# Kernel tuning notes

Measured on AMD Instinct MI355X. Metric: run time of the kernel, lower is better.

Reference implementation:

```python
import jax, jax.numpy as jnp
import numpy as np

B, T, IN = 32, 1024, 256
H = 128          # hidden_size
NL = 2           # num_layers
NC = 4           # num_classes
F2 = 2 * H       # bidirectional feature size


def _lstm_dir(xs, w_ih, w_hh, b_ih, b_hh, reverse):
    # xs: [T, B, in]; w_ih: [4H, in]; w_hh: [4H, H]
    if reverse:
        xs = xs[::-1]
    h0 = jnp.zeros((xs.shape[1], H), xs.dtype)
    c0 = jnp.zeros((xs.shape[1], H), xs.dtype)

    def step(carry, xt):
        h, c = carry
        g = xt @ w_ih.T + b_ih + h @ w_hh.T + b_hh  # [B, 4H]
        i, f, gg, o = jnp.split(g, 4, axis=-1)       # PyTorch gate order i,f,g,o
        c = jax.nn.sigmoid(f) * c + jax.nn.sigmoid(i) * jnp.tanh(gg)
        h = jax.nn.sigmoid(o) * jnp.tanh(c)
        return (h, c), h

    _, hs = jax.lax.scan(step, (h0, c0), xs)  # [T, B, H]
    if reverse:
        hs = hs[::-1]
    return hs


def setup_inputs() -> dict:
    key = jax.random.key(0)
    ks = jax.random.split(key, 12)
    s = 0.05
    x = jax.random.normal(ks[0], (B, T, IN), jnp.float32)
    # stacked LSTM params: [layer, direction, ...]; layer0 in = IN, layer1 in = 2H = IN
    w_ih = jax.random.normal(ks[1], (NL, 2, 4 * H, IN), jnp.float32) * s
    w_hh = jax.random.normal(ks[2], (NL, 2, 4 * H, H), jnp.float32) * s
    b_ih = jax.random.normal(ks[3], (NL, 2, 4 * H), jnp.float32) * s
    b_hh = jax.random.normal(ks[4], (NL, 2, 4 * H), jnp.float32) * s
    wq = jax.random.normal(ks[5], (F2, F2), jnp.float32) * s
    wk = jax.random.normal(ks[6], (F2, F2), jnp.float32) * s
    wv = jax.random.normal(ks[7], (F2, F2), jnp.float32) * s
    bq = jax.random.normal(ks[8], (F2,), jnp.float32) * s
    bk = jax.random.normal(ks[9], (F2,), jnp.float32) * s
    bv = jax.random.normal(ks[10], (F2,), jnp.float32) * s
    w_fc = jax.random.normal(ks[11], (NC, F2), jnp.float32) * s
    b_fc = jnp.zeros((NC,), jnp.float32)
    return {"x": x, "w_ih": w_ih, "w_hh": w_hh, "b_ih": b_ih, "b_hh": b_hh,
            "wq": wq, "wk": wk, "wv": wv, "bq": bq, "bk": bk, "bv": bv,
            "w_fc": w_fc, "b_fc": b_fc}


def reference(x, w_ih, w_hh, b_ih, b_hh, wq, wk, wv, bq, bk, bv, w_fc, b_fc):
    # --- biLSTM (eval mode: inter-layer dropout inactive) ---
    xs = jnp.swapaxes(x, 0, 1)  # time-major [T, B, IN]
    for l in range(NL):
        fwd = _lstm_dir(xs, w_ih[l, 0], w_hh[l, 0], b_ih[l, 0], b_hh[l, 0], False)
        bwd = _lstm_dir(xs, w_ih[l, 1], w_hh[l, 1], b_ih[l, 1], b_hh[l, 1], True)
        xs = jnp.concatenate([fwd, bwd], axis=-1)  # [T, B, 2H]
    out = jnp.swapaxes(xs, 0, 1)  # [B, T, 2H]
    # --- naive full self-attention ---
    q = out @ wq.T + bq
    k = out @ wk.T + bk
    v = out @ wv.T + bv
    scores = jnp.einsum('btd,bsd->bts', q, k) / jnp.sqrt(jnp.float32(F2))
    attn = jax.nn.softmax(scores, axis=-1)          # [B, T, T]
    ctx = jnp.einsum('bts,bsd->btd', attn, v)       # [B, T, 2H]
    # --- FC head on last timestep ---
    return ctx[:, -1, :] @ w_fc.T + b_fc            # [B, NC]
```

## Files before the change

kernel.cpp:

```cpp
#include <hip/hip_runtime.h>
#include <math.h>
#include <stdint.h>

#define BB 32
#define TT 1024
#define HH 128
#define G4 512
#define CH 16
#define XPS 516

typedef _Float16 half2_t __attribute__((ext_vector_type(2)));
typedef _Float16 half8_t __attribute__((ext_vector_type(8)));
typedef float f32x4 __attribute__((ext_vector_type(4)));

__device__ __forceinline__ float fdot2f(half2_t a, half2_t b, float c) {
    return __builtin_amdgcn_fdot2(a, b, c, false);
}
__device__ __forceinline__ float rcpf(float x) {
    return __builtin_amdgcn_rcpf(x);
}
__device__ __forceinline__ float dpp_xor1(float x) {
    return __builtin_bit_cast(float, __builtin_amdgcn_update_dpp(
        0, __builtin_bit_cast(int, x), 0xB1, 0xF, 0xF, true));
}
__device__ __forceinline__ float dpp_xor2(float x) {
    return __builtin_bit_cast(float, __builtin_amdgcn_update_dpp(
        0, __builtin_bit_cast(int, x), 0x4E, 0xF, 0xF, true));
}
__device__ __forceinline__ void bar_lgkm() {
    asm volatile("s_waitcnt lgkmcnt(0)\n\ts_barrier" ::: "memory");
}

__global__ __launch_bounds__(256) void cvt_wih(
    const float* __restrict__ w, _Float16* __restrict__ o)
{
    const int i = (blockIdx.x * 256 + threadIdx.x) * 4;
    float4 f = *(const float4*)(w + i);
    half2_t t[2] = { half2_t{(_Float16)f.x, (_Float16)f.y},
                     half2_t{(_Float16)f.z, (_Float16)f.w} };
    *(float2*)(o + i) = *(float2*)t;
}

__global__ __launch_bounds__(512, 1) void lstm_fused(
    const float* __restrict__ x_in,
    const _Float16* __restrict__ wih16_l,
    const float* __restrict__ b_ih_l,
    const float* __restrict__ b_hh_l,
    const float* __restrict__ w_hh_l,
    float* __restrict__ out)
{
    const int b = blockIdx.x & 31;
    const int d = blockIdx.x >> 5;
    const int tid = threadIdx.x;
    const int wvid = tid >> 6;
    const int l = tid & 63;
    const int s = l & 3;
    const int g = l >> 2;
    const int j = (wvid << 4) | g;

    __shared__ __align__(16) _Float16 hs[HH];
    __shared__ __align__(16) float xp[2][CH * XPS];
    __shared__ __align__(16) half2_t xr[2][CH * 128];
    __shared__ __align__(16) float obuf[CH * HH];

    half2_t wv[4][16];
#pragma unroll
    for (int G = 0; G < 4; ++G) {
        const float* wr = w_hh_l + (size_t)(d * G4 + 128 * G + j) * HH + 32 * s;
#pragma unroll
        for (int q4 = 0; q4 < 8; ++q4) {
            float4 f = *(const float4*)(wr + 4 * q4);
            wv[G][2 * q4]     = half2_t{(_Float16)f.x, (_Float16)f.y};
            wv[G][2 * q4 + 1] = half2_t{(_Float16)f.z, (_Float16)f.w};
        }
    }

    const int acol0 = wvid * 64 + (l & 15);
    const _Float16* wn = wih16_l + ((size_t)d * G4 + acol0) * 256 + (l >> 4) * 8;
    const float bias0 = b_ih_l[d * G4 + acol0]      + b_hh_l[d * G4 + acol0];
    const float bias1 = b_ih_l[d * G4 + acol0 + 16] + b_hh_l[d * G4 + acol0 + 16];
    const float bias2 = b_ih_l[d * G4 + acol0 + 32] + b_hh_l[d * G4 + acol0 + 32];
    const float bias3 = b_ih_l[d * G4 + acol0 + 48] + b_hh_l[d * G4 + acol0 + 48];

    const int cbase = ((acol0 & 127) << 2) + (acol0 >> 7);

    const float* xbase = x_in + (size_t)b * TT * 256;

    const int a_noswz = (l & 15) * 512 + (l >> 4) * 16;
    const int a_swz   = (l & 7) << 4;
    const int w_swz_byte = (tid * 16) ^ (((tid >> 5) & 7) << 4);

#pragma unroll 1
    for (int p = 0; p < 2; ++p) {
        const int tlo = d ? (1008 - p * CH) : p * CH;
        const float* gs = xbase + (size_t)tlo * 256 + tid * 8;
        float4 f0 = *(const float4*)gs;
        float4 f1 = *(const float4*)(gs + 4);
        half2_t t4[4] = { half2_t{(_Float16)f0.x, (_Float16)f0.y},
                          half2_t{(_Float16)f0.z, (_Float16)f0.w},
                          half2_t{(_Float16)f1.x, (_Float16)f1.y},
                          half2_t{(_Float16)f1.z, (_Float16)f1.w} };
        *(float4*)((char*)xr[p] + w_swz_byte) = *(float4*)t4;
    }
    __syncthreads();

    f32x4 acc0 = {bias0, bias0, bias0, bias0};
    f32x4 acc1 = {bias1, bias1, bias1, bias1};
    f32x4 acc2 = {bias2, bias2, bias2, bias2};
    f32x4 acc3 = {bias3, bias3, bias3, bias3};

#pragma unroll
    for (int kt = 0; kt < 8; ++kt) {
        half8_t af = *(const half8_t*)((const char*)xr[0] + ((a_noswz + kt * 64) ^ a_swz));
        acc0 = __builtin_amdgcn_mfma_f32_16x16x32_f16(af, *(const half8_t*)(wn +         kt * 32), acc0, 0, 0, 0);
        acc1 = __builtin_amdgcn_mfma_f32_16x16x32_f16(af, *(const half8_t*)(wn +  4096 + kt * 32), acc1, 0, 0, 0);
        acc2 = __builtin_amdgcn_mfma_f32_16x16x32_f16(af, *(const half8_t*)(wn +  8192 + kt * 32), acc2, 0, 0, 0);
        acc3 = __builtin_amdgcn_mfma_f32_16x16x32_f16(af, *(const half8_t*)(wn + 12288 + kt * 32), acc3, 0, 0, 0);
    }
    {
        const int rb = (l >> 4) * 4;
#pragma unroll
        for (int q = 0; q < 4; ++q) {
            const int ix = (rb + q) * XPS + cbase;
            xp[0][ix]       = acc0[q];
            xp[0][ix + 64]  = acc1[q];
            xp[0][ix + 128] = acc2[q];
            xp[0][ix + 192] = acc3[q];
        }
    }
    acc0 = (f32x4){bias0, bias0, bias0, bias0};
    acc1 = (f32x4){bias1, bias1, bias1, bias1};
    acc2 = (f32x4){bias2, bias2, bias2, bias2};
    acc3 = (f32x4){bias3, bias3, bias3, bias3};

    if (tid < 64) ((half2_t*)hs)[tid] = half2_t{(_Float16)0.f, (_Float16)0.f};
    float c = 0.f;
    float* ob = out + (size_t)b * TT * 256 + d * HH;
    __syncthreads();

    float4 rg0 = {}, rg1 = {};
    for (int ck = 0; ck < 64; ++ck) {
        const int cur = ck & 1;
        const bool doproj = (ck + 1 < 64);
        if (ck + 2 < 64) {
            const int tlo2 = d ? (1008 - (ck + 2) * CH) : (ck + 2) * CH;
            const float* gs = xbase + (size_t)tlo2 * 256 + tid * 8;
            rg0 = *(const float4*)gs;
            rg1 = *(const float4*)(gs + 4);
        }
        const float* xb = xp[cur];
        const char* xr_rd = (const char*)xr[cur ^ 1];

        auto rec_step = [&](int si) {
            const int lds_t = d ? (CH - 1 - si) : si;
            const float4 xg4 = *(const float4*)&xb[lds_t * XPS + (j << 2)];

            const float4* hp = (const float4*)(hs + 32 * s);
            float4 hA = hp[0], hB = hp[1], hC = hp[2], hD = hp[3];
            half2_t hh[16];
            hh[0]  = __builtin_bit_cast(half2_t, hA.x);
            hh[1]  = __builtin_bit_cast(half2_t, hA.y);
            hh[2]  = __builtin_bit_cast(half2_t, hA.z);
            hh[3]  = __builtin_bit_cast(half2_t, hA.w);
            hh[4]  = __builtin_bit_cast(half2_t, hB.x);
            hh[5]  = __builtin_bit_cast(half2_t, hB.y);
            hh[6]  = __builtin_bit_cast(half2_t, hB.z);
            hh[7]  = __builtin_bit_cast(half2_t, hB.w);
            hh[8]  = __builtin_bit_cast(half2_t, hC.x);
            hh[9]  = __builtin_bit_cast(half2_t, hC.y);
            hh[10] = __builtin_bit_cast(half2_t, hC.z);
            hh[11] = __builtin_bit_cast(half2_t, hC.w);
            hh[12] = __builtin_bit_cast(half2_t, hD.x);
            hh[13] = __builtin_bit_cast(half2_t, hD.y);
            hh[14] = __builtin_bit_cast(half2_t, hD.z);
            hh[15] = __builtin_bit_cast(half2_t, hD.w);

            float a0 = 0.f, a1 = 0.f, a2 = 0.f, a3 = 0.f;
            float e0 = 0.f, e1 = 0.f, e2 = 0.f, e3 = 0.f;
#pragma unroll
            for (int kk = 0; kk < 8; ++kk) {
                a0 = fdot2f(wv[0][kk], hh[kk], a0);
                a1 = fdot2f(wv[1][kk], hh[kk], a1);
                a2 = fdot2f(wv[2][kk], hh[kk], a2);
                a3 = fdot2f(wv[3][kk], hh[kk], a3);
                e0 = fdot2f(wv[0][kk + 8], hh[kk + 8], e0);
                e1 = fdot2f(wv[1][kk + 8], hh[kk + 8], e1);
                e2 = fdot2f(wv[2][kk + 8], hh[kk + 8], e2);
                e3 = fdot2f(wv[3][kk + 8], hh[kk + 8], e3);
            }
            a0 += e0; a1 += e1; a2 += e2; a3 += e3;

            a0 += dpp_xor1(a0); a0 += dpp_xor2(a0);
            a1 += dpp_xor1(a1); a1 += dpp_xor2(a1);
            a2 += dpp_xor1(a2); a2 += dpp_xor2(a2);
            a3 += dpp_xor1(a3); a3 += dpp_xor2(a3);

            const float gi = rcpf(1.f + __expf(-(a0 + xg4.x)));
            const float gf = rcpf(1.f + __expf(-(a1 + xg4.y)));
            const float gg = 1.f - 2.f * rcpf(1.f + __expf(2.f * (a2 + xg4.z)));
            const float go = rcpf(1.f + __expf(-(a3 + xg4.w)));
            c = gf * c + gi * gg;
            const float th = 1.f - 2.f * rcpf(1.f + __expf(2.f * c));
            const float h = go * th;
            if (s == 0) {
                hs[j] = (_Float16)h;
                obuf[si * HH + j] = h;
            }
        };

        half8_t gbEA = {}, gbEB = {}, gbOA = {}, gbOB = {};
        if (doproj) {
            gbEA = *(const half8_t*)(wn);
            gbEB = *(const half8_t*)(wn + 4096);
        }

#pragma unroll 1
        for (int sp = 0; sp < CH / 2; ++sp) {
            const int kt = sp;
            half8_t afrag = {};
            if (doproj) {
                afrag = *(const half8_t*)(xr_rd + ((a_noswz + kt * 64) ^ a_swz));
                gbOA = *(const half8_t*)(wn +  8192 + kt * 32);
                gbOB = *(const half8_t*)(wn + 12288 + kt * 32);
            }
            rec_step(2 * sp);
            if (doproj) {
                acc0 = __builtin_amdgcn_mfma_f32_16x16x32_f16(afrag, gbEA, acc0, 0, 0, 0);
                acc1 = __builtin_amdgcn_mfma_f32_16x16x32_f16(afrag, gbEB, acc1, 0, 0, 0);
            }
            bar_lgkm();
            if (doproj) {
                const int ktn = (kt + 1) & 7;
                gbEA = *(const half8_t*)(wn +        ktn * 32);
                gbEB = *(const half8_t*)(wn + 4096 + ktn * 32);
            }
            rec_step(2 * sp + 1);
            if (doproj) {
                acc2 = __builtin_amdgcn_mfma_f32_16x16x32_f16(afrag, gbOA, acc2, 0, 0, 0);
                acc3 = __builtin_amdgcn_mfma_f32_16x16x32_f16(afrag, gbOB, acc3, 0, 0, 0);
            }
            bar_lgkm();
        }

        {
            const int idx = tid * 4;
            const int sf = idx >> 7, jf = idx & 127;
            const int sg = ck * CH + sf;
            const int t  = d ? (TT - 1 - sg) : sg;
            float4 o0 = *(const float4*)&obuf[idx];
            *(float4*)&ob[(size_t)t * 256 + jf] = o0;
        }
        if (doproj) {
            float* xpn = xp[cur ^ 1];
            const int rb = (l >> 4) * 4;
#pragma unroll
            for (int q = 0; q < 4; ++q) {
                const int ix = (rb + q) * XPS + cbase;
                xpn[ix]       = acc0[q];
                xpn[ix + 64]  = acc1[q];
                xpn[ix + 128] = acc2[q];
                xpn[ix + 192] = acc3[q];
            }
            acc0 = (f32x4){bias0, bias0, bias0, bias0};
            acc1 = (f32x4){bias1, bias1, bias1, bias1};
            acc2 = (f32x4){bias2, bias2, bias2, bias2};
            acc3 = (f32x4){bias3, bias3, bias3, bias3};
        }
        if (ck + 2 < 64) {
            half2_t t4[4] = { half2_t{(_Float16)rg0.x, (_Float16)rg0.y},
                              half2_t{(_Float16)rg0.z, (_Float16)rg0.w},
                              half2_t{(_Float16)rg1.x, (_Float16)rg1.y},
                              half2_t{(_Float16)rg1.z, (_Float16)rg1.w} };
            *(float4*)((char*)xr[cur] + w_swz_byte) = *(float4*)t4;
        }
        __syncthreads();
    }
}


__global__ __launch_bounds__(256) void attn_qr(
    const float* __restrict__ out1, const float* __restrict__ wq,
    const float* __restrict__ bq,   const float* __restrict__ wk,
    float* __restrict__ r_ws, float* __restrict__ ctxw, float* __restrict__ den)
{
    const int b = blockIdx.x;
    const int tid = threadIdx.x;
    __shared__ float xl[256], q[256];
    const float* ob = out1 + (size_t)b * TT * 256;

    xl[tid] = ob[(size_t)(TT - 1) * 256 + tid];
    ctxw[b * 256 + tid] = 0.f;
    if (tid == 0) den[b] = 0.f;
    __syncthreads();

    float acc = bq[tid];
    const float* wqr = wq + (size_t)tid * 256;
#pragma unroll 4
    for (int k = 0; k < 256; ++k) acc += xl[k] * wqr[k];
    q[tid] = acc;
    __syncthreads();

    acc = 0.f;
#pragma unroll 4
    for (int dd = 0; dd < 256; ++dd) acc += q[dd] * wk[(size_t)dd * 256 + tid];
    r_ws[b * 256 + tid] = acc * 0.0625f;
}

__global__ __launch_bounds__(256) void attn_sc(
    const float* __restrict__ out1, const float* __restrict__ r_ws,
    float* __restrict__ ctxw, float* __restrict__ den)
{
    const int b  = blockIdx.x >> 3;
    const int s8 = blockIdx.x & 7;
    const int tid = threadIdx.x;
    __shared__ __align__(16) float r[256];
    __shared__ float ev[128];
    __shared__ float red[256];

    const float* ob = out1 + (size_t)b * TT * 256 + (size_t)s8 * 128 * 256;
    r[tid] = r_ws[b * 256 + tid];
    __syncthreads();

    const int wave = tid >> 6, lane = tid & 63;
    float4 r4 = *(const float4*)&r[lane * 4];
    for (int t = wave; t < 128; t += 4) {
        float4 o4 = *(const float4*)(ob + (size_t)t * 256 + lane * 4);
        float p = r4.x * o4.x + r4.y * o4.y + r4.z * o4.z + r4.w * o4.w;
#pragma unroll
        for (int off = 32; off > 0; off >>= 1) p += __shfl_down(p, off, 64);
        if (lane == 0) ev[t] = expf(p);
    }
    __syncthreads();

    red[tid] = (tid < 128) ? ev[tid] : 0.f;
    __syncthreads();
    for (int st = 128; st > 0; st >>= 1) {
        if (tid < st) red[tid] += red[tid + st];
        __syncthreads();
    }
    if (tid == 0) atomicAdd(&den[b], red[0]);

    float a = 0.f;
#pragma unroll 4
    for (int t = 0; t < 128; ++t) a += ev[t] * ob[(size_t)t * 256 + tid];
    atomicAdd(&ctxw[b * 256 + tid], a);
}

__global__ __launch_bounds__(256) void attn_fc(
    const float* __restrict__ ctxw, const float* __restrict__ den,
    const float* __restrict__ wv,   const float* __restrict__ bv,
    const float* __restrict__ wfc,  const float* __restrict__ bfc,
    float* __restrict__ outp)
{
    const int b = blockIdx.x;
    const int tid = threadIdx.x;
    __shared__ float u[256], cx[256];

    u[tid] = ctxw[b * 256 + tid] / den[b];
    __syncthreads();

    float acc = bv[tid];
    const float* wr = wv + (size_t)tid * 256;
#pragma unroll 4
    for (int k = 0; k < 256; ++k) acc += u[k] * wr[k];
    cx[tid] = acc;
    __syncthreads();

    if (tid < 4) {
        float o = bfc[tid];
        for (int k = 0; k < 256; ++k) o += cx[k] * wfc[tid * 256 + k];
        outp[b * 4 + tid] = o;
    }
}

extern "C" void kernel_launch(void* const* d_in, const int* in_sizes, int n_in,
                              void* d_out, int out_size, void* d_ws, size_t ws_size,
                              hipStream_t stream)
{
    const float* x    = (const float*)d_in[0];
    const float* w_ih = (const float*)d_in[1];
    const float* w_hh = (const float*)d_in[2];
    const float* b_ih = (const float*)d_in[3];
    const float* b_hh = (const float*)d_in[4];
    const float* wq   = (const float*)d_in[5];
    const float* wk   = (const float*)d_in[6];
    const float* wv   = (const float*)d_in[7];
    const float* bq   = (const float*)d_in[8];
    const float* bv   = (const float*)d_in[10];
    const float* wfc  = (const float*)d_in[11];
    const float* bfcv = (const float*)d_in[12];
    float* outp = (float*)d_out;

    float* ws = (float*)d_ws;
    _Float16* wih16 = (_Float16*)ws;
    float* out0 = ws + 262144;
    float* out1 = out0 + 8388608;
    float* r_ws = out1 + 8388608;
    float* ctxw = r_ws + 8192;
    float* den  = ctxw + 8192;

    cvt_wih<<<512, 256, 0, stream>>>(w_ih, wih16);

    lstm_fused<<<64, 512, 0, stream>>>(x, wih16, b_ih, b_hh, w_hh, out0);
    lstm_fused<<<64, 512, 0, stream>>>(out0, wih16 + 262144, b_ih + 1024, b_hh + 1024,
                                       w_hh + 2 * 512 * 128, out1);

    attn_qr<<<32, 256, 0, stream>>>(out1, wq, bq, wk, r_ws, ctxw, den);
    attn_sc<<<256, 256, 0, stream>>>(out1, r_ws, ctxw, den);
    attn_fc<<<32, 256, 0, stream>>>(ctxw, den, wv, bv, wfc, bfcv, outp);
}
```

Before: 1.679 ms.

## Fuse attention kernels into one launch with last-block completion counter

Merges the three attention kernels (query/key projection, score+weighted sum, value/FC head) into a single kernel. Each of the 8 blocks per batch recomputes the q·Wk vector redundantly, and the last block to finish, detected via an atomic counter, runs the value projection and FC head. Zero-initialisation of the accumulators moves into the weight conversion kernel. This removes two kernel launches and their gaps, at the cost of 8x redundant projection work per batch and reliance on threadfence/atomic ordering.

```diff
diff --git a/kernel.cpp b/kernel.cpp
--- a/kernel.cpp
+++ b/kernel.cpp
@@ -32,13 +32,16 @@
 }
 
 __global__ __launch_bounds__(256) void cvt_wih(
-    const float* __restrict__ w, _Float16* __restrict__ o)
+    const float* __restrict__ w, _Float16* __restrict__ o,
+    float* __restrict__ ctxw, float* __restrict__ den, int* __restrict__ cnt)
 {
     const int i = (blockIdx.x * 256 + threadIdx.x) * 4;
     float4 f = *(const float4*)(w + i);
     half2_t t[2] = { half2_t{(_Float16)f.x, (_Float16)f.y},
                      half2_t{(_Float16)f.z, (_Float16)f.w} };
     *(float2*)(o + i) = *(float2*)t;
+    if (blockIdx.x < 32) ctxw[blockIdx.x * 256 + threadIdx.x] = 0.f;
+    if (blockIdx.x == 32 && threadIdx.x < 32) { den[threadIdx.x] = 0.f; cnt[threadIdx.x] = 0; }
 }
 
 __global__ __launch_bounds__(512, 1) void lstm_fused(
@@ -277,58 +280,51 @@
     }
 }
 
-
-__global__ __launch_bounds__(256) void attn_qr(
-    const float* __restrict__ out1, const float* __restrict__ wq,
-    const float* __restrict__ bq,   const float* __restrict__ wk,
-    float* __restrict__ r_ws, float* __restrict__ ctxw, float* __restrict__ den)
+__global__ __launch_bounds__(256) void attn_all(
+    const float* __restrict__ out1,
+    const float* __restrict__ wq, const float* __restrict__ bq,
+    const float* __restrict__ wk,
+    const float* __restrict__ wv, const float* __restrict__ bv,
+    const float* __restrict__ wfc, const float* __restrict__ bfc,
+    float* __restrict__ ctxw, float* __restrict__ den, int* __restrict__ cnt,
+    float* __restrict__ outp)
 {
-    const int b = blockIdx.x;
+    const int b  = blockIdx.x >> 3;
+    const int s8 = blockIdx.x & 7;
     const int tid = threadIdx.x;
     __shared__ float xl[256], q[256];
-    const float* ob = out1 + (size_t)b * TT * 256;
-
-    xl[tid] = ob[(size_t)(TT - 1) * 256 + tid];
-    ctxw[b * 256 + tid] = 0.f;
-    if (tid == 0) den[b] = 0.f;
-    __syncthreads();
-
+    __shared__ __align__(16) float r[256];
+    __shared__ float ev[128];
+    __shared__ float red[256];
+    __shared__ int lastflag;
+
+    const float* obase = out1 + (size_t)b * TT * 256;
+
+    xl[tid] = obase[(size_t)(TT - 1) * 256 + tid];
+    __syncthreads();
     float acc = bq[tid];
     const float* wqr = wq + (size_t)tid * 256;
 #pragma unroll 4
     for (int k = 0; k < 256; ++k) acc += xl[k] * wqr[k];
     q[tid] = acc;
     __syncthreads();
-
     acc = 0.f;
 #pragma unroll 4
     for (int dd = 0; dd < 256; ++dd) acc += q[dd] * wk[(size_t)dd * 256 + tid];
-    r_ws[b * 256 + tid] = acc * 0.0625f;
-}
-
-__global__ __launch_bounds__(256) void attn_sc(
-    const float* __restrict__ out1, const float* __restrict__ r_ws,
-    float* __restrict__ ctxw, float* __restrict__ den)
-{
-    const int b  = blockIdx.x >> 3;
-    const int s8 = blockIdx.x & 7;
-    const int tid = threadIdx.x;
-    __shared__ __align__(16) float r[256];
-    __shared__ float ev[128];
-    __shared__ float red[256];
-
-    const float* ob = out1 + (size_t)b * TT * 256 + (size_t)s8 * 128 * 256;
-    r[tid] = r_ws[b * 256 + tid];
-    __syncthreads();
-
-    const int wave = tid >> 6, lane = tid & 63;
-    float4 r4 = *(const float4*)&r[lane * 4];
-    for (int t = wave; t < 128; t += 4) {
-        float4 o4 = *(const float4*)(ob + (size_t)t * 256 + lane * 4);
-        float p = r4.x * o4.x + r4.y * o4.y + r4.z * o4.z + r4.w * o4.w;
-#pragma unroll
-        for (int off = 32; off > 0; off >>= 1) p += __shfl_down(p, off, 64);
-        if (lane == 0) ev[t] = expf(p);
+    r[tid] = acc * 0.0625f;
+    __syncthreads();
+
+    const float* ob = obase + (size_t)s8 * 128 * 256;
+    {
+        const int wave = tid >> 6, lane = tid & 63;
+        float4 r4 = *(const float4*)&r[lane * 4];
+        for (int t = wave; t < 128; t += 4) {
+            float4 o4 = *(const float4*)(ob + (size_t)t * 256 + lane * 4);
+            float p = r4.x * o4.x + r4.y * o4.y + r4.z * o4.z + r4.w * o4.w;
+#pragma unroll
+            for (int off = 32; off > 0; off >>= 1) p += __shfl_down(p, off, 64);
+            if (lane == 0) ev[t] = expf(p);
+        }
     }
     __syncthreads();
 
@@ -340,35 +336,38 @@
     }
     if (tid == 0) atomicAdd(&den[b], red[0]);
 
-    float a = 0.f;
+    acc = 0.f;
 #pragma unroll 4
-    for (int t = 0; t < 128; ++t) a += ev[t] * ob[(size_t)t * 256 + tid];
-    atomicAdd(&ctxw[b * 256 + tid], a);
-}
-
-__global__ __launch_bounds__(256) void attn_fc(
-    const float* __restrict__ ctxw, const float* __restrict__ den,
-    const float* __restrict__ wv,   const float* __restrict__ bv,
-    const float* __restrict__ wfc,  const float* __restrict__ bfc,
-    float* __restrict__ outp)
-{
-    const int b = blockIdx.x;
-    const int tid = threadIdx.x;
-    __shared__ float u[256], cx[256];
-
-    u[tid] = ctxw[b * 256 + tid] / den[b];
-    __syncthreads();
-
-    float acc = bv[tid];
+    for (int t = 0; t < 128; ++t) acc += ev[t] * ob[(size_t)t * 256 + tid];
+    atomicAdd(&ctxw[b * 256 + tid], acc);
+
+    __syncthreads();
+    if (tid == 0) {
+        __threadfence();
+        const int prev = atomicAdd(&cnt[b], 1);
+        lastflag = (prev == 7);
+    }
+    __syncthreads();
+    if (!lastflag) return;
+
+    __threadfence();
+    if (tid == 0) red[0] = atomicAdd(&den[b], 0.f);
+    const float uu = atomicAdd(&ctxw[b * 256 + tid], 0.f);
+    __syncthreads();
+    const float inv = 1.f / red[0];
+    xl[tid] = uu * inv;
+    __syncthreads();
+
+    acc = bv[tid];
     const float* wr = wv + (size_t)tid * 256;
 #pragma unroll 4
-    for (int k = 0; k < 256; ++k) acc += u[k] * wr[k];
-    cx[tid] = acc;
+    for (int k = 0; k < 256; ++k) acc += xl[k] * wr[k];
+    q[tid] = acc;
     __syncthreads();
 
     if (tid < 4) {
         float o = bfc[tid];
-        for (int k = 0; k < 256; ++k) o += cx[k] * wfc[tid * 256 + k];
+        for (int k = 0; k < 256; ++k) o += q[k] * wfc[tid * 256 + k];
         outp[b * 4 + tid] = o;
     }
 }
@@ -395,17 +394,16 @@
     _Float16* wih16 = (_Float16*)ws;
     float* out0 = ws + 262144;
     float* out1 = out0 + 8388608;
-    float* r_ws = out1 + 8388608;
-    float* ctxw = r_ws + 8192;
+    float* ctxw = out1 + 8388608;
     float* den  = ctxw + 8192;
-
-    cvt_wih<<<512, 256, 0, stream>>>(w_ih, wih16);
+    int*   cnt  = (int*)(den + 32);
+
+    cvt_wih<<<512, 256, 0, stream>>>(w_ih, wih16, ctxw, den, cnt);
 
     lstm_fused<<<64, 512, 0, stream>>>(x, wih16, b_ih, b_hh, w_hh, out0);
     lstm_fused<<<64, 512, 0, stream>>>(out0, wih16 + 262144, b_ih + 1024, b_hh + 1024,
                                        w_hh + 2 * 512 * 128, out1);
 
-    attn_qr<<<32, 256, 0, stream>>>(out1, wq, bq, wk, r_ws, ctxw, den);
-    attn_sc<<<256, 256, 0, stream>>>(out1, r_ws, ctxw, den);
-    attn_fc<<<32, 256, 0, stream>>>(ctxw, den, wv, bv, wfc, bfcv, outp);
-}
+    attn_all<<<256, 256, 0, stream>>>(out1, wq, bq, wk, wv, bv, wfc, bfcv,
+                                      ctxw, den, cnt, outp);
+}
```

New measurement: 1.696 ms. Within noise of the previous version (+1.0%).
